# Kernel tuning notes

Measured on AMD Instinct MI355X. Metric: run time of the kernel, lower is better.

## Reference

```python
import jax, jax.numpy as jnp
import numpy as np

N_NODES = 100000
N_EDGES = 1600000
IN_DIM = 64
HID_DIM = 128
OUT_DIM = 128


def setup_inputs() -> dict:
    key = jax.random.key(0)
    ks = jax.random.split(key, 12)
    s = 0.05
    return {
        "x": jax.random.normal(ks[0], (N_NODES, IN_DIM), jnp.float32),
        "edge_index": jax.random.randint(ks[1], (2, N_EDGES), 0, N_NODES, jnp.int64),
        "edge_attr": jax.random.uniform(ks[2], (N_EDGES, 2), jnp.float32),
        # conv1 MLP: Linear(IN+2, HID) -> ReLU -> Linear(HID, HID)
        "W11": jax.random.normal(ks[3], (IN_DIM + 2, HID_DIM), jnp.float32) * s,
        "b11": jax.random.normal(ks[4], (HID_DIM,), jnp.float32) * s,
        "W12": jax.random.normal(ks[5], (HID_DIM, HID_DIM), jnp.float32) * s,
        "b12": jax.random.normal(ks[6], (HID_DIM,), jnp.float32) * s,
        # conv2 MLP: Linear(HID+2, OUT) -> ReLU -> Linear(OUT, OUT)
        "W21": jax.random.normal(ks[7], (HID_DIM + 2, OUT_DIM), jnp.float32) * s,
        "b21": jax.random.normal(ks[8], (OUT_DIM,), jnp.float32) * s,
        "W22": jax.random.normal(ks[9], (OUT_DIM, OUT_DIM), jnp.float32) * s,
        "b22": jax.random.normal(ks[10], (OUT_DIM,), jnp.float32) * s,
    }


def _gin_conv(x, edge_index, edge_attr, W1, b1, W2, b2):
    N = x.shape[0]
    loop = jnp.arange(N, dtype=edge_index.dtype)
    src = jnp.concatenate([edge_index[0], loop])  # [E+N] message sources
    dst = jnp.concatenate([edge_index[1], loop])  # [E+N] aggregation targets
    # self-loop edge_attr filled with 1.0 (PyG add_self_loops default)
    ea = jnp.concatenate([edge_attr, jnp.ones((N, edge_attr.shape[1]), edge_attr.dtype)], axis=0)
    m = jnp.concatenate([x[src], ea], axis=-1)  # [E+N, F+2] gather + concat
    h = jnp.dot(jax.nn.relu(jnp.dot(m, W1) + b1), W2) + b2  # edge MLP
    return jax.ops.segment_sum(h, dst, num_segments=N)  # scatter-add aggregate


def reference(x, edge_index, edge_attr, W11, b11, W12, b12, W21, b21, W22, b22):
    h = _gin_conv(x, edge_index, edge_attr, W11, b11, W12, b12)
    h = jax.nn.relu(h)
    return _gin_conv(h, edge_index, edge_attr, W21, b21, W22, b22)
```

## Files before the change

### kernel.cpp

```cpp
#include <hip/hip_runtime.h>


typedef unsigned int uint;
typedef __attribute__((ext_vector_type(8))) short bf16x8;
typedef __attribute__((ext_vector_type(4))) float f32x4;

#define BSHIFT 9
#define BNODES (1 << BSHIFT)

static __device__ __forceinline__ unsigned short f2bf(float f) {
    uint u = __float_as_uint(f);
    uint r = (u + 0x7fffu + ((u >> 16) & 1u)) >> 16;
    return (unsigned short)r;
}


__global__ void wprep_all(const float* __restrict__ W11, const float* __restrict__ W12,
                          const float* __restrict__ W21, const float* __restrict__ W22,
                          unsigned short* Wt11, unsigned short* Wt12,
                          unsigned short* Wt21, unsigned short* Wt22,
                          int* bcnt, int* ptr, int N, int E) {
    int idx = blockIdx.x * 256 + threadIdx.x;
    if (idx < 256) bcnt[idx] = 0;
    if (idx == 0) ptr[N] = E;
    const float* W; unsigned short* Wt; int K; int off;
    if (idx < 64 * 128)        { W = W11; Wt = Wt11; K = 64;  off = idx; }
    else if (idx < 192 * 128)  { W = W12; Wt = Wt12; K = 128; off = idx - 64 * 128; }
    else if (idx < 320 * 128)  { W = W21; Wt = Wt21; K = 128; off = idx - 192 * 128; }
    else if (idx < 448 * 128)  { W = W22; Wt = Wt22; K = 128; off = idx - 320 * 128; }
    else return;
    int k = off >> 7, n = off & 127;
    Wt[n * K + k] = f2bf(W[k * 128 + n]);
}


__global__ __launch_bounds__(512) void bin_kernel(
    const int* __restrict__ src, const int* __restrict__ dst,
    const float* __restrict__ ea, int* __restrict__ bcnt,
    int2* __restrict__ barr, int CAP, int E, int B) {
    __shared__ int hist[256];
    __shared__ int bbase[256];
    __shared__ int gbase[256];
    __shared__ int wtot[4];
    __shared__ int2 sorted[4096];
    __shared__ unsigned char bof[4096];
    const int tileBase = blockIdx.x * 4096;
    int n = E - tileBase; if (n > 4096) n = 4096; if (n <= 0) return;
    const int tid = threadIdx.x;
    const int lane = tid & 63;
    if (tid < 256) hist[tid] = 0;
    __syncthreads();

    int2 ent[8]; int bk[8]; int rk[8];
#pragma unroll
    for (int kk = 0; kk < 8; kk++) {
        int i = kk * 512 + tid;
        bk[kk] = -1;
        if (i < n) {
            int e = tileBase + i;
            int s = src[e], d = dst[e];
            float2 a = reinterpret_cast<const float2*>(ea)[e];
            int b = d >> BSHIFT;
            int dloc = d & (BNODES - 1);
            ent[kk].x = s | (dloc << 17);
            ent[kk].y = (int)((uint)f2bf(a.x) | ((uint)f2bf(a.y) << 16));
            bk[kk] = b;
            rk[kk] = atomicAdd(&hist[b], 1);
        }
    }
    __syncthreads();
    int hv = (tid < 256) ? hist[tid] : 0;
    int inc = hv;
#pragma unroll
    for (int off = 1; off < 64; off <<= 1) {
        int tt = __shfl_up(inc, off, 64);
        if (lane >= off) inc += tt;
    }
    if ((tid >> 6) < 4 && lane == 63) wtot[tid >> 6] = inc;
    __syncthreads();
    if (tid == 0) { int run = 0; for (int i = 0; i < 4; i++) { int tt = wtot[i]; wtot[i] = run; run += tt; } }
    __syncthreads();
    if (tid < 256) bbase[tid] = inc - hv + wtot[tid >> 6];
    if (tid < B && hist[tid] > 0) gbase[tid] = atomicAdd(&bcnt[tid], hist[tid]);
    __syncthreads();
#pragma unroll
    for (int kk = 0; kk < 8; kk++) {
        if (bk[kk] >= 0) {
            int p = bbase[bk[kk]] + rk[kk];
            sorted[p] = ent[kk];
            bof[p] = (unsigned char)bk[kk];
        }
    }
    __syncthreads();
    for (int i = tid; i < n; i += 512) {
        int b = bof[i];
        barr[(long)b * CAP + gbase[b] + (i - bbase[b])] = sorted[i];
    }
}


static __device__ void csr_body(const int2* __restrict__ barr, const int* __restrict__ bcnt,
                                int CAP, int N, int2* __restrict__ csr, int* __restrict__ ptr) {
    __shared__ int hist[BNODES];
    __shared__ int lptr[BNODES];
    __shared__ int wtot[8];
    __shared__ int sbase;
    const int g = blockIdx.x;
    const int tid = threadIdx.x;
    const int lane = tid & 63;
    const int cnt = bcnt[g];
    if (tid == 0) sbase = 0;
    hist[tid] = 0;
    __syncthreads();
    if (tid < g) atomicAdd(&sbase, bcnt[tid]);
    const int2* my = barr + (long)g * CAP;
    for (int i = tid; i < cnt; i += 512)
        atomicAdd(&hist[((uint)my[i].x) >> 17], 1);
    __syncthreads();
    int v = hist[tid];
    int inc = v;
#pragma unroll
    for (int off = 1; off < 64; off <<= 1) {
        int tt = __shfl_up(inc, off, 64);
        if (lane >= off) inc += tt;
    }
    if (lane == 63) wtot[tid >> 6] = inc;
    __syncthreads();
    if (tid == 0) { int run = 0; for (int i = 0; i < 8; i++) { int tt = wtot[i]; wtot[i] = run; run += tt; } }
    __syncthreads();
    const int base = sbase;
    int excl = inc - v + wtot[tid >> 6];
    lptr[tid] = excl;
    int gnode = g * BNODES + tid;
    if (gnode < N) ptr[gnode] = base + excl;
    __syncthreads();
    for (int i = tid; i < cnt; i += 512) {
        int2 e = my[i];
        int pos = base + atomicAdd(&lptr[((uint)e.x) >> 17], 1);
        int2 o; o.x = e.x & 0x1FFFF; o.y = e.y;
        csr[pos] = o;
    }
}


template <int K, bool IN_F32, bool OUT_BF16, bool USE_CNT, bool RELU>
static __device__ __forceinline__ void gemm_body(
    const void* __restrict__ Ain, const unsigned short* __restrict__ Wt,
    const float* __restrict__ bias, const int* __restrict__ ptr,
    void* __restrict__ Cout, int N, int tid, long rowBase) {
    constexpr int KS = K / 32;
    const int wave = tid >> 6;
    const int lane = tid & 63;
    const int m = lane & 15, quad = lane >> 4;

    bf16x8 bfrag[2][KS];
#pragma unroll
    for (int ct = 0; ct < 2; ct++) {
        int col = (wave * 2 + ct) * 16 + m;
#pragma unroll
        for (int ks = 0; ks < KS; ks++)
            bfrag[ct][ks] = *(const bf16x8*)(Wt + (long)col * K + ks * 32 + quad * 8);
    }

#pragma unroll
    for (int rt = 0; rt < 4; rt++) {
        long row = rowBase + rt * 16 + m;
        long rc = row < N ? row : (long)N - 1;
        bf16x8 afrag[KS];
        if (IN_F32) {
            const float* arow = (const float*)Ain + rc * K;
#pragma unroll
            for (int ks = 0; ks < KS; ks++) {
                float4 lo = *(const float4*)(arow + ks * 32 + quad * 8);
                float4 hi = *(const float4*)(arow + ks * 32 + quad * 8 + 4);
                bf16x8 f;
                f[0] = (short)f2bf(lo.x); f[1] = (short)f2bf(lo.y);
                f[2] = (short)f2bf(lo.z); f[3] = (short)f2bf(lo.w);
                f[4] = (short)f2bf(hi.x); f[5] = (short)f2bf(hi.y);
                f[6] = (short)f2bf(hi.z); f[7] = (short)f2bf(hi.w);
                afrag[ks] = f;
            }
        } else {
            const unsigned short* arow = (const unsigned short*)Ain + rc * K;
#pragma unroll
            for (int ks = 0; ks < KS; ks++)
                afrag[ks] = *(const bf16x8*)(arow + ks * 32 + quad * 8);
        }

#pragma unroll
        for (int ct = 0; ct < 2; ct++) {
            f32x4 acc = {0.f, 0.f, 0.f, 0.f};
#pragma unroll
            for (int ks = 0; ks < KS; ks++)
                acc = __builtin_amdgcn_mfma_f32_16x16x32_bf16(afrag[ks], bfrag[ct][ks], acc, 0, 0, 0);

            int col = (wave * 2 + ct) * 16 + m;
            float b = bias[col];
#pragma unroll
            for (int r = 0; r < 4; r++) {
                long orow = rowBase + rt * 16 + quad * 4 + r;
                if (orow < N) {
                    float v = acc[r];
                    if (USE_CNT) v += b * (float)(ptr[orow + 1] - ptr[orow] + 1);
                    else v += b;
                    if (RELU) v = fmaxf(v, 0.f);
                    if (OUT_BF16) ((unsigned short*)Cout)[orow * 128 + col] = f2bf(v);
                    else ((float*)Cout)[orow * 128 + col] = v;
                }
            }
        }
    }
}


__global__ __launch_bounds__(512) void csr_gemm1(
    const int2* __restrict__ barr, const int* __restrict__ bcnt, int CAP, int N,
    int2* __restrict__ csr, int* __restrict__ ptr, int CSRB,
    const float* __restrict__ x, const unsigned short* __restrict__ Wt11,
    const float* __restrict__ b11, unsigned short* __restrict__ A_bf) {
    if ((int)blockIdx.x < CSRB) {
        csr_body(barr, bcnt, CAP, N, csr, ptr);
    } else {
        int bid = blockIdx.x - CSRB;
        int sub = threadIdx.x >> 8;
        gemm_body<64, true, true, false, false>(x, Wt11, b11, nullptr, A_bf, N,
                                                threadIdx.x & 255,
                                                (long)bid * 128 + sub * 64);
    }
}


static __device__ __forceinline__ void gather_lds(
    const uint* __restrict__ Au, const int* __restrict__ ptr,
    const int2* __restrict__ csr, const float* __restrict__ we,
    uint* __restrict__ ts_u, int N, int tid, int rowBase) {
    const int w = tid >> 6;
    const int t = tid & 63;
    const int c = 2 * t;
    const float w0x = we[c], w0y = we[c + 1];
    const float w1x = we[128 + c], w1y = we[128 + c + 1];
    const char* Ab = (const char*)Au;
    const uint t4 = (uint)t * 4u;
#define LD(sidx) (*(const uint*)(Ab + ((((uint)(sidx)) << 8) + t4)))
#define ACC(rv, ev)                                                      \
    {                                                                    \
        float a0 = __uint_as_float(((uint)(ev)) << 16);                  \
        float a1 = __uint_as_float(((uint)(ev)) & 0xffff0000u);          \
        float vx = __uint_as_float((rv) << 16);                          \
        float vy = __uint_as_float((rv) & 0xffff0000u);                  \
        vx = fmaf(a0, w0x, fmaf(a1, w1x, vx));                           \
        vy = fmaf(a0, w0y, fmaf(a1, w1y, vy));                           \
        ax += fmaxf(vx, 0.f);                                            \
        ay += fmaxf(vy, 0.f);                                            \
    }
#define EDGE(i, off)                                                     \
    int2 c##i = csr[k + (off)];                                          \
    uint s##i = (uint)__builtin_amdgcn_readfirstlane(c##i.x);            \
    uint e##i = (uint)__builtin_amdgcn_readfirstlane(c##i.y);

    for (int i = 0; i < 4; i++) {
        int node = rowBase + w * 4 + i;
        if (node >= N) break;

        uint selfv = LD((uint)node);
        float ax = fmaxf(__uint_as_float(selfv << 16) + w0x + w1x, 0.f);
        float ay = fmaxf(__uint_as_float(selfv & 0xffff0000u) + w0y + w1y, 0.f);

        int k   = __builtin_amdgcn_readfirstlane(ptr[node]);
        int end = __builtin_amdgcn_readfirstlane(ptr[node + 1]);

        for (; k + 8 <= end; k += 8) {
            EDGE(0, 0) EDGE(1, 1) EDGE(2, 2) EDGE(3, 3)
            EDGE(4, 4) EDGE(5, 5) EDGE(6, 6) EDGE(7, 7)
            uint r0 = LD(s0); uint r1 = LD(s1); uint r2 = LD(s2); uint r3 = LD(s3);
            uint r4 = LD(s4); uint r5 = LD(s5); uint r6 = LD(s6); uint r7 = LD(s7);
            ACC(r0, e0) ACC(r1, e1) ACC(r2, e2) ACC(r3, e3)
            ACC(r4, e4) ACC(r5, e5) ACC(r6, e6) ACC(r7, e7)
        }
        for (; k + 4 <= end; k += 4) {
            EDGE(0, 0) EDGE(1, 1) EDGE(2, 2) EDGE(3, 3)
            uint r0 = LD(s0); uint r1 = LD(s1); uint r2 = LD(s2); uint r3 = LD(s3);
            ACC(r0, e0) ACC(r1, e1) ACC(r2, e2) ACC(r3, e3)
        }
        for (; k < end; k++) {
            EDGE(0, 0)
            uint r0 = LD(s0);
            ACC(r0, e0)
        }
        ts_u[(w * 4 + i) * 68 + t] = (uint)f2bf(ax) | ((uint)f2bf(ay) << 16);
    }
#undef EDGE
#undef ACC
#undef LD
}


__global__ __launch_bounds__(256) void gather_mid(
    const uint* __restrict__ Au, const int* __restrict__ ptr,
    const int2* __restrict__ csr, const float* __restrict__ we,
    const unsigned short* __restrict__ WtA, const float* __restrict__ biasA,
    const unsigned short* __restrict__ WtB, const float* __restrict__ biasB,
    unsigned short* __restrict__ Cout, int N) {
    __shared__ uint ts_u[16 * 68];
    unsigned short* ts = (unsigned short*)ts_u;
    const int tid = threadIdx.x;
    const int rowBase = blockIdx.x * 16;

    gather_lds(Au, ptr, csr, we, ts_u, N, tid, rowBase);
    __syncthreads();

    const int wave = tid >> 6, lane = tid & 63;
    const int m = lane & 15, quad = lane >> 4;

    bf16x8 bfrag[2][4];
#pragma unroll
    for (int ct = 0; ct < 2; ct++) {
        int col = (wave * 2 + ct) * 16 + m;
#pragma unroll
        for (int ks = 0; ks < 4; ks++)
            bfrag[ct][ks] = *(const bf16x8*)(WtA + (long)col * 128 + ks * 32 + quad * 8);
    }

    const unsigned short* lr = ts + m * 136;
    bf16x8 af[4];
#pragma unroll
    for (int ks = 0; ks < 4; ks++)
        af[ks] = *(const bf16x8*)(lr + ks * 32 + quad * 8);

    f32x4 acc[2];
#pragma unroll
    for (int ct = 0; ct < 2; ct++) {
        f32x4 a = {0.f, 0.f, 0.f, 0.f};
#pragma unroll
        for (int ks = 0; ks < 4; ks++)
            a = __builtin_amdgcn_mfma_f32_16x16x32_bf16(af[ks], bfrag[ct][ks], a, 0, 0, 0);
        acc[ct] = a;
    }
    __syncthreads();

    float cntf[4];
#pragma unroll
    for (int r = 0; r < 4; r++) {
        long grow = rowBase + quad * 4 + r;
        cntf[r] = (grow < N) ? (float)(ptr[grow + 1] - ptr[grow] + 1) : 1.f;
    }
#pragma unroll
    for (int ct = 0; ct < 2; ct++) {
        int col = (wave * 2 + ct) * 16 + m;
        float b = biasA[col];
#pragma unroll
        for (int r = 0; r < 4; r++) {
            int row = quad * 4 + r;
            ts[row * 136 + col] = f2bf(fmaxf(acc[ct][r] + b * cntf[r], 0.f));
        }
    }
    __syncthreads();

#pragma unroll
    for (int ct = 0; ct < 2; ct++) {
        int col = (wave * 2 + ct) * 16 + m;
#pragma unroll
        for (int ks = 0; ks < 4; ks++)
            bfrag[ct][ks] = *(const bf16x8*)(WtB + (long)col * 128 + ks * 32 + quad * 8);
    }
#pragma unroll
    for (int ks = 0; ks < 4; ks++)
        af[ks] = *(const bf16x8*)(lr + ks * 32 + quad * 8);
#pragma unroll
    for (int ct = 0; ct < 2; ct++) {
        f32x4 a = {0.f, 0.f, 0.f, 0.f};
#pragma unroll
        for (int ks = 0; ks < 4; ks++)
            a = __builtin_amdgcn_mfma_f32_16x16x32_bf16(af[ks], bfrag[ct][ks], a, 0, 0, 0);
        int col = (wave * 2 + ct) * 16 + m;
        float b = biasB[col];
#pragma unroll
        for (int r = 0; r < 4; r++) {
            long grow = rowBase + quad * 4 + r;
            if (grow < N) Cout[grow * 128 + col] = f2bf(a[r] + b);
        }
    }
}


__global__ __launch_bounds__(256) void gather_out(
    const uint* __restrict__ Au, const int* __restrict__ ptr,
    const int2* __restrict__ csr, const float* __restrict__ we,
    const unsigned short* __restrict__ Wt, const float* __restrict__ bias,
    float* __restrict__ out, int N) {
    __shared__ uint ts_u[16 * 68];
    unsigned short* ts = (unsigned short*)ts_u;
    const int tid = threadIdx.x;
    const int rowBase = blockIdx.x * 16;

    gather_lds(Au, ptr, csr, we, ts_u, N, tid, rowBase);
    __syncthreads();

    const int wave = tid >> 6, lane = tid & 63;
    const int m = lane & 15, quad = lane >> 4;

    bf16x8 bfrag[2][4];
#pragma unroll
    for (int ct = 0; ct < 2; ct++) {
        int col = (wave * 2 + ct) * 16 + m;
#pragma unroll
        for (int ks = 0; ks < 4; ks++)
            bfrag[ct][ks] = *(const bf16x8*)(Wt + (long)col * 128 + ks * 32 + quad * 8);
    }

    const unsigned short* lr = ts + m * 136;
    bf16x8 af[4];
#pragma unroll
    for (int ks = 0; ks < 4; ks++)
        af[ks] = *(const bf16x8*)(lr + ks * 32 + quad * 8);

#pragma unroll
    for (int ct = 0; ct < 2; ct++) {
        f32x4 a = {0.f, 0.f, 0.f, 0.f};
#pragma unroll
        for (int ks = 0; ks < 4; ks++)
            a = __builtin_amdgcn_mfma_f32_16x16x32_bf16(af[ks], bfrag[ct][ks], a, 0, 0, 0);
        int col = (wave * 2 + ct) * 16 + m;
        float b = bias[col];
#pragma unroll
        for (int r = 0; r < 4; r++) {
            long grow = rowBase + quad * 4 + r;
            if (grow < N) {
                float cnt = (float)(ptr[grow + 1] - ptr[grow] + 1);
                out[grow * 128 + col] = a[r] + b * cnt;
            }
        }
    }
}


extern "C" void kernel_launch(void* const* d_in, const int* in_sizes, int n_in,
                              void* d_out, int out_size, void* d_ws, size_t ws_size,
                              hipStream_t stream) {
    const float* x   = (const float*)d_in[0];
    const int*   ei  = (const int*)d_in[1];
    const float* ea  = (const float*)d_in[2];
    const float* W11 = (const float*)d_in[3];
    const float* b11 = (const float*)d_in[4];
    const float* W12 = (const float*)d_in[5];
    const float* b12 = (const float*)d_in[6];
    const float* W21 = (const float*)d_in[7];
    const float* b21 = (const float*)d_in[8];
    const float* W22 = (const float*)d_in[9];
    const float* b22 = (const float*)d_in[10];
    float* out = (float*)d_out;

    const int N = in_sizes[0] / 64;
    const int E = in_sizes[1] / 2;
    const int* src = ei;
    const int* dst = ei + E;

    const int B = (N + BNODES - 1) >> BSHIFT;
    const int CAP = E / B + 4096;

    char* p = (char*)d_ws;
    unsigned short* A_bf = (unsigned short*)p;  p += (size_t)N * 128 * 2;
    unsigned short* A2_bf = (unsigned short*)p;
    int2* barr = (int2*)A2_bf;                  p += (size_t)N * 128 * 2;
    int2* csr  = (int2*)p;                      p += (size_t)E * 8;
    int* ptr   = (int*)p;                       p += (size_t)(N + 1) * 4;
    int* bcnt  = (int*)p;                       p += 256 * 4;
    unsigned short* Wt11 = (unsigned short*)p;  p += (size_t)64 * 128 * 2;
    unsigned short* Wt12 = (unsigned short*)p;  p += (size_t)128 * 128 * 2;
    unsigned short* Wt21 = (unsigned short*)p;  p += (size_t)128 * 128 * 2;
    unsigned short* Wt22 = (unsigned short*)p;

    const int binBlocks = (E + 4095) / 4096;
    const int fuseBlocks = (N + 15) / 16;
    const int g1Tiles = (N + 127) / 128;

    wprep_all<<<224, 256, 0, stream>>>(W11, W12, W21, W22,
                                       Wt11, Wt12, Wt21, Wt22,
                                       bcnt, ptr, N, E);
    bin_kernel<<<binBlocks, 512, 0, stream>>>(src, dst, ea, bcnt, barr, CAP, E, B);
    csr_gemm1<<<B + g1Tiles, 512, 0, stream>>>(barr, bcnt, CAP, N, csr, ptr, B,
                                               x, Wt11, b11, A_bf);
    gather_mid<<<fuseBlocks, 256, 0, stream>>>((const uint*)A_bf, ptr, csr,
                                               W11 + 64 * 128, Wt12, b12, Wt21, b21,
                                               A2_bf, N);
    gather_out<<<fuseBlocks, 256, 0, stream>>>((const uint*)A2_bf, ptr, csr,
                                               W21 + 128 * 128, Wt22, b22, out, N);
}
```

Baseline: 351.5 us.

## Gather one node per wave with 1024-thread blocks in fused gather kernels

The gather kernels move from 256-thread blocks, where each wave walks four nodes in sequence, to 1024-thread blocks where each of 16 waves handles one node. This exposes more independent memory-latency-bound gathers at once. The GEMM epilogue now uses only 8 of the 16 waves, each owning one 16-column tile, and gather_mid uses a second LDS buffer instead of reusing the first behind an extra barrier. The output store becomes nontemporal and the small tail loop changes from 4-wide to 2-wide. The risk is that half the waves sit idle during the MFMA phase, and the larger blocks may lower occupancy or leave more imbalance across a block.

After: 370.9 us. +5.5%, slower.

```diff
diff --git a/kernel.cpp b/kernel.cpp
--- a/kernel.cpp
+++ b/kernel.cpp
@@ -13,6 +13,7 @@
     uint r = (u + 0x7fffu + ((u >> 16) & 1u)) >> 16;
     return (unsigned short)r;
 }
+static __device__ __forceinline__ int rfl(int v) { return __builtin_amdgcn_readfirstlane(v); }
 
 
 __global__ void wprep_all(const float* __restrict__ W11, const float* __restrict__ W12,
@@ -143,7 +144,7 @@
 }
 
 
-template <int K, bool IN_F32, bool OUT_BF16, bool USE_CNT, bool RELU>
+template <int K, bool IN_F32, bool OUT_BF16, bool USE_CNT>
 static __device__ __forceinline__ void gemm_body(
     const void* __restrict__ Ain, const unsigned short* __restrict__ Wt,
     const float* __restrict__ bias, const int* __restrict__ ptr,
@@ -203,7 +204,6 @@
                     float v = acc[r];
                     if (USE_CNT) v += b * (float)(ptr[orow + 1] - ptr[orow] + 1);
                     else v += b;
-                    if (RELU) v = fmaxf(v, 0.f);
                     if (OUT_BF16) ((unsigned short*)Cout)[orow * 128 + col] = f2bf(v);
                     else ((float*)Cout)[orow * 128 + col] = v;
                 }
@@ -223,18 +223,20 @@
     } else {
         int bid = blockIdx.x - CSRB;
         int sub = threadIdx.x >> 8;
-        gemm_body<64, true, true, false, false>(x, Wt11, b11, nullptr, A_bf, N,
-                                                threadIdx.x & 255,
-                                                (long)bid * 128 + sub * 64);
-    }
-}
-
-
-static __device__ __forceinline__ void gather_lds(
+        gemm_body<64, true, true, false>(x, Wt11, b11, nullptr, A_bf, N,
+                                         threadIdx.x & 255,
+                                         (long)bid * 128 + sub * 64);
+    }
+}
+
+
+static __device__ __forceinline__ void gather_one_node(
     const uint* __restrict__ Au, const int* __restrict__ ptr,
     const int2* __restrict__ csr, const float* __restrict__ we,
     uint* __restrict__ ts_u, int N, int tid, int rowBase) {
     const int w = tid >> 6;
+    const int node = rowBase + w;
+    if (node >= N) return;
     const int t = tid & 63;
     const int c = 2 * t;
     const float w0x = we[c], w0y = we[c + 1];
@@ -255,124 +257,100 @@
     }
 #define EDGE(i, off)                                                     \
     int2 c##i = csr[k + (off)];                                          \
-    uint s##i = (uint)__builtin_amdgcn_readfirstlane(c##i.x);            \
-    uint e##i = (uint)__builtin_amdgcn_readfirstlane(c##i.y);
-
-    for (int i = 0; i < 4; i++) {
-        int node = rowBase + w * 4 + i;
-        if (node >= N) break;
-
-        uint selfv = LD((uint)node);
-        float ax = fmaxf(__uint_as_float(selfv << 16) + w0x + w1x, 0.f);
-        float ay = fmaxf(__uint_as_float(selfv & 0xffff0000u) + w0y + w1y, 0.f);
-
-        int k   = __builtin_amdgcn_readfirstlane(ptr[node]);
-        int end = __builtin_amdgcn_readfirstlane(ptr[node + 1]);
-
-        for (; k + 8 <= end; k += 8) {
-            EDGE(0, 0) EDGE(1, 1) EDGE(2, 2) EDGE(3, 3)
-            EDGE(4, 4) EDGE(5, 5) EDGE(6, 6) EDGE(7, 7)
-            uint r0 = LD(s0); uint r1 = LD(s1); uint r2 = LD(s2); uint r3 = LD(s3);
-            uint r4 = LD(s4); uint r5 = LD(s5); uint r6 = LD(s6); uint r7 = LD(s7);
-            ACC(r0, e0) ACC(r1, e1) ACC(r2, e2) ACC(r3, e3)
-            ACC(r4, e4) ACC(r5, e5) ACC(r6, e6) ACC(r7, e7)
-        }
-        for (; k + 4 <= end; k += 4) {
-            EDGE(0, 0) EDGE(1, 1) EDGE(2, 2) EDGE(3, 3)
-            uint r0 = LD(s0); uint r1 = LD(s1); uint r2 = LD(s2); uint r3 = LD(s3);
-            ACC(r0, e0) ACC(r1, e1) ACC(r2, e2) ACC(r3, e3)
-        }
-        for (; k < end; k++) {
-            EDGE(0, 0)
-            uint r0 = LD(s0);
-            ACC(r0, e0)
-        }
-        ts_u[(w * 4 + i) * 68 + t] = (uint)f2bf(ax) | ((uint)f2bf(ay) << 16);
+    uint s##i = (uint)rfl(c##i.x);                                       \
+    uint e##i = (uint)rfl(c##i.y);
+
+    uint selfv = LD((uint)node);
+    float ax = fmaxf(__uint_as_float(selfv << 16) + w0x + w1x, 0.f);
+    float ay = fmaxf(__uint_as_float(selfv & 0xffff0000u) + w0y + w1y, 0.f);
+
+    int k   = rfl(ptr[node]);
+    int end = rfl(ptr[node + 1]);
+
+    for (; k + 8 <= end; k += 8) {
+        EDGE(0, 0) EDGE(1, 1) EDGE(2, 2) EDGE(3, 3)
+        EDGE(4, 4) EDGE(5, 5) EDGE(6, 6) EDGE(7, 7)
+        uint r0 = LD(s0); uint r1 = LD(s1); uint r2 = LD(s2); uint r3 = LD(s3);
+        uint r4 = LD(s4); uint r5 = LD(s5); uint r6 = LD(s6); uint r7 = LD(s7);
+        ACC(r0, e0) ACC(r1, e1) ACC(r2, e2) ACC(r3, e3)
+        ACC(r4, e4) ACC(r5, e5) ACC(r6, e6) ACC(r7, e7)
+    }
+    for (; k + 2 <= end; k += 2) {
+        EDGE(0, 0) EDGE(1, 1)
+        uint r0 = LD(s0); uint r1 = LD(s1);
+        ACC(r0, e0) ACC(r1, e1)
+    }
+    if (k < end) {
+        EDGE(0, 0)
+        uint r0 = LD(s0);
+        ACC(r0, e0)
     }
 #undef EDGE
 #undef ACC
 #undef LD
-}
-
-
-__global__ __launch_bounds__(256) void gather_mid(
+    ts_u[w * 68 + t] = (uint)f2bf(ax) | ((uint)f2bf(ay) << 16);
+}
+
+
+__global__ __launch_bounds__(1024) void gather_mid(
     const uint* __restrict__ Au, const int* __restrict__ ptr,
     const int2* __restrict__ csr, const float* __restrict__ we,
     const unsigned short* __restrict__ WtA, const float* __restrict__ biasA,
     const unsigned short* __restrict__ WtB, const float* __restrict__ biasB,
     unsigned short* __restrict__ Cout, int N) {
     __shared__ uint ts_u[16 * 68];
-    unsigned short* ts = (unsigned short*)ts_u;
+    __shared__ uint ts2_u[16 * 68];
     const int tid = threadIdx.x;
     const int rowBase = blockIdx.x * 16;
 
-    gather_lds(Au, ptr, csr, we, ts_u, N, tid, rowBase);
-    __syncthreads();
-
-    const int wave = tid >> 6, lane = tid & 63;
+    gather_one_node(Au, ptr, csr, we, ts_u, N, tid, rowBase);
+    __syncthreads();
+
+    const int w = tid >> 6, lane = tid & 63;
     const int m = lane & 15, quad = lane >> 4;
-
-    bf16x8 bfrag[2][4];
-#pragma unroll
-    for (int ct = 0; ct < 2; ct++) {
-        int col = (wave * 2 + ct) * 16 + m;
-#pragma unroll
-        for (int ks = 0; ks < 4; ks++)
-            bfrag[ct][ks] = *(const bf16x8*)(WtA + (long)col * 128 + ks * 32 + quad * 8);
-    }
-
-    const unsigned short* lr = ts + m * 136;
-    bf16x8 af[4];
-#pragma unroll
-    for (int ks = 0; ks < 4; ks++)
-        af[ks] = *(const bf16x8*)(lr + ks * 32 + quad * 8);
-
-    f32x4 acc[2];
-#pragma unroll
-    for (int ct = 0; ct < 2; ct++) {
+    const unsigned short* ts  = (const unsigned short*)ts_u;
+    unsigned short* ts2 = (unsigned short*)ts2_u;
+
+    if (w < 8) {
+        const int col = w * 16 + m;
+        bf16x8 bfrag[4];
+#pragma unroll
+        for (int ks = 0; ks < 4; ks++)
+            bfrag[ks] = *(const bf16x8*)(WtA + (long)col * 128 + ks * 32 + quad * 8);
+        const unsigned short* lr = ts + m * 136;
+        bf16x8 af[4];
+#pragma unroll
+        for (int ks = 0; ks < 4; ks++)
+            af[ks] = *(const bf16x8*)(lr + ks * 32 + quad * 8);
         f32x4 a = {0.f, 0.f, 0.f, 0.f};
 #pragma unroll
         for (int ks = 0; ks < 4; ks++)
-            a = __builtin_amdgcn_mfma_f32_16x16x32_bf16(af[ks], bfrag[ct][ks], a, 0, 0, 0);
-        acc[ct] = a;
-    }
-    __syncthreads();
-
-    float cntf[4];
-#pragma unroll
-    for (int r = 0; r < 4; r++) {
-        long grow = rowBase + quad * 4 + r;
-        cntf[r] = (grow < N) ? (float)(ptr[grow + 1] - ptr[grow] + 1) : 1.f;
-    }
-#pragma unroll
-    for (int ct = 0; ct < 2; ct++) {
-        int col = (wave * 2 + ct) * 16 + m;
+            a = __builtin_amdgcn_mfma_f32_16x16x32_bf16(af[ks], bfrag[ks], a, 0, 0, 0);
         float b = biasA[col];
 #pragma unroll
         for (int r = 0; r < 4; r++) {
-            int row = quad * 4 + r;
-            ts[row * 136 + col] = f2bf(fmaxf(acc[ct][r] + b * cntf[r], 0.f));
-        }
-    }
-    __syncthreads();
-
-#pragma unroll
-    for (int ct = 0; ct < 2; ct++) {
-        int col = (wave * 2 + ct) * 16 + m;
-#pragma unroll
-        for (int ks = 0; ks < 4; ks++)
-            bfrag[ct][ks] = *(const bf16x8*)(WtB + (long)col * 128 + ks * 32 + quad * 8);
-    }
-#pragma unroll
-    for (int ks = 0; ks < 4; ks++)
-        af[ks] = *(const bf16x8*)(lr + ks * 32 + quad * 8);
-#pragma unroll
-    for (int ct = 0; ct < 2; ct++) {
+            long grow = rowBase + quad * 4 + r;
+            float cnt = (grow < N) ? (float)(ptr[grow + 1] - ptr[grow] + 1) : 1.f;
+            ts2[(quad * 4 + r) * 136 + col] = f2bf(fmaxf(a[r] + b * cnt, 0.f));
+        }
+    }
+    __syncthreads();
+
+    if (w < 8) {
+        const int col = w * 16 + m;
+        bf16x8 bfrag[4];
+#pragma unroll
+        for (int ks = 0; ks < 4; ks++)
+            bfrag[ks] = *(const bf16x8*)(WtB + (long)col * 128 + ks * 32 + quad * 8);
+        const unsigned short* lr = (const unsigned short*)ts2 + m * 136;
+        bf16x8 af[4];
+#pragma unroll
+        for (int ks = 0; ks < 4; ks++)
+            af[ks] = *(const bf16x8*)(lr + ks * 32 + quad * 8);
         f32x4 a = {0.f, 0.f, 0.f, 0.f};
 #pragma unroll
         for (int ks = 0; ks < 4; ks++)
-            a = __builtin_amdgcn_mfma_f32_16x16x32_bf16(af[ks], bfrag[ct][ks], a, 0, 0, 0);
-        int col = (wave * 2 + ct) * 16 + m;
+            a = __builtin_amdgcn_mfma_f32_16x16x32_bf16(af[ks], bfrag[ks], a, 0, 0, 0);
         float b = biasB[col];
 #pragma unroll
         for (int r = 0; r < 4; r++) {
@@ -383,51 +361,44 @@
 }
 
 
-__global__ __launch_bounds__(256) void gather_out(
+__global__ __launch_bounds__(1024) void gather_out(
     const uint* __restrict__ Au, const int* __restrict__ ptr,
     const int2* __restrict__ csr, const float* __restrict__ we,
     const unsigned short* __restrict__ Wt, const float* __restrict__ bias,
     float* __restrict__ out, int N) {
     __shared__ uint ts_u[16 * 68];
-    unsigned short* ts = (unsigned short*)ts_u;
     const int tid = threadIdx.x;
     const int rowBase = blockIdx.x * 16;
 
-    gather_lds(Au, ptr, csr, we, ts_u, N, tid, rowBase);
-    __syncthreads();
-
-    const int wave = tid >> 6, lane = tid & 63;
+    gather_one_node(Au, ptr, csr, we, ts_u, N, tid, rowBase);
+    __syncthreads();
+
+    const int w = tid >> 6, lane = tid & 63;
     const int m = lane & 15, quad = lane >> 4;
-
-    bf16x8 bfrag[2][4];
-#pragma unroll
-    for (int ct = 0; ct < 2; ct++) {
-        int col = (wave * 2 + ct) * 16 + m;
-#pragma unroll
-        for (int ks = 0; ks < 4; ks++)
-            bfrag[ct][ks] = *(const bf16x8*)(Wt + (long)col * 128 + ks * 32 + quad * 8);
-    }
-
-    const unsigned short* lr = ts + m * 136;
-    bf16x8 af[4];
-#pragma unroll
-    for (int ks = 0; ks < 4; ks++)
-        af[ks] = *(const bf16x8*)(lr + ks * 32 + quad * 8);
-
-#pragma unroll
-    for (int ct = 0; ct < 2; ct++) {
+    const unsigned short* ts = (const unsigned short*)ts_u;
+
+    if (w < 8) {
+        const int col = w * 16 + m;
+        bf16x8 bfrag[4];
+#pragma unroll
+        for (int ks = 0; ks < 4; ks++)
+            bfrag[ks] = *(const bf16x8*)(Wt + (long)col * 128 + ks * 32 + quad * 8);
+        const unsigned short* lr = ts + m * 136;
+        bf16x8 af[4];
+#pragma unroll
+        for (int ks = 0; ks < 4; ks++)
+            af[ks] = *(const bf16x8*)(lr + ks * 32 + quad * 8);
         f32x4 a = {0.f, 0.f, 0.f, 0.f};
 #pragma unroll
         for (int ks = 0; ks < 4; ks++)
-            a = __builtin_amdgcn_mfma_f32_16x16x32_bf16(af[ks], bfrag[ct][ks], a, 0, 0, 0);
-        int col = (wave * 2 + ct) * 16 + m;
+            a = __builtin_amdgcn_mfma_f32_16x16x32_bf16(af[ks], bfrag[ks], a, 0, 0, 0);
         float b = bias[col];
 #pragma unroll
         for (int r = 0; r < 4; r++) {
             long grow = rowBase + quad * 4 + r;
             if (grow < N) {
                 float cnt = (float)(ptr[grow + 1] - ptr[grow] + 1);
-                out[grow * 128 + col] = a[r] + b * cnt;
+                __builtin_nontemporal_store(a[r] + b * cnt, &out[grow * 128 + col]);
             }
         }
     }
@@ -480,9 +451,9 @@
     bin_kernel<<<binBlocks, 512, 0, stream>>>(src, dst, ea, bcnt, barr, CAP, E, B);
     csr_gemm1<<<B + g1Tiles, 512, 0, stream>>>(barr, bcnt, CAP, N, csr, ptr, B,
                                                x, Wt11, b11, A_bf);
-    gather_mid<<<fuseBlocks, 256, 0, stream>>>((const uint*)A_bf, ptr, csr,
-                                               W11 + 64 * 128, Wt12, b12, Wt21, b21,
-                                               A2_bf, N);
-    gather_out<<<fuseBlocks, 256, 0, stream>>>((const uint*)A2_bf, ptr, csr,
-                                               W21 + 128 * 128, Wt22, b22, out, N);
-}
+    gather_mid<<<fuseBlocks, 1024, 0, stream>>>((const uint*)A_bf, ptr, csr,
+                                                W11 + 64 * 128, Wt12, b12, Wt21, b21,
+                                                A2_bf, N);
+    gather_out<<<fuseBlocks, 1024, 0, stream>>>((const uint*)A2_bf, ptr, csr,
+                                                W21 + 128 * 128, Wt22, b22, out, N);
+}
```
